# Kernel tuning notes

Measured on AMD Instinct MI355X. Metric: run time of the kernel, lower is better.

Reference implementation:

```python
import jax, jax.numpy as jnp
import numpy as np

D_MODEL = 4096
D_FIBER = 16
D_CONTROL = 64
EMA_MOMENTUM = 0.9


def setup_inputs() -> dict:
    key = jax.random.key(0)
    k_h, k_f, k_w1, k_w2 = jax.random.split(key, 4)
    B, S = 4, 2048
    hidden = jax.random.normal(k_h, (B, S, D_MODEL), dtype=jnp.float32)
    # torch nn.Linear stores weight as [out, in]; fiber_proj init: normal std=0.02
    W_fiber = jax.random.normal(k_f, (D_FIBER, D_MODEL), dtype=jnp.float32) * 0.02
    # predictor[0]: Linear(d_model+d_fiber, d_control) with default torch init (uniform)
    fan_in1 = D_MODEL + D_FIBER
    bound1 = 1.0 / np.sqrt(fan_in1)
    W1 = jax.random.uniform(k_w1, (D_CONTROL, fan_in1), dtype=jnp.float32, minval=-bound1, maxval=bound1)
    b1 = jnp.zeros((D_CONTROL,), dtype=jnp.float32)
    # predictor[-2]: Linear(d_control, 1), weight normal std=0.01, bias zero
    W2 = jax.random.normal(k_w2, (1, D_CONTROL), dtype=jnp.float32) * 0.01
    b2 = jnp.zeros((1,), dtype=jnp.float32)
    lam = jnp.asarray(1.0, dtype=jnp.float32)
    return {"hidden": hidden, "W_fiber": W_fiber, "W1": W1, "b1": b1, "W2": W2, "b2": b2, "lam": lam}


def _causal_ema(delta_h, alpha):
    # h_t = alpha*h_{t-1} + (1-alpha)*d_t, h_{-1} = 0. delta_h: [B,S]
    B = delta_h.shape[0]
    def step(h_prev, d_t):
        h_t = alpha * h_prev + (1.0 - alpha) * d_t
        return h_t, h_t
    _, hs = jax.lax.scan(step, jnp.zeros((B,), delta_h.dtype), jnp.swapaxes(delta_h, 0, 1))
    return jnp.swapaxes(hs, 0, 1)  # [B,S]


def reference(hidden, W_fiber, W1, b1, W2, b2, lam):
    h = hidden.astype(jnp.float32)                      # [B,S,D]
    fiber = jnp.einsum('bsd,fd->bsf', h, W_fiber)       # [B,S,16]
    combined = jnp.concatenate([h, fiber], axis=-1)     # [B,S,D+16]
    z = jax.nn.gelu(jnp.einsum('bsc,kc->bsk', combined, W1) + b1, approximate=False)
    delta_h = jax.nn.softplus(jnp.einsum('bsk,ok->bso', z, W2) + b2)[..., 0]  # [B,S]
    field = _causal_ema(delta_h, EMA_MOMENTUM)          # [B,S]
    gate = jax.nn.sigmoid(-lam * field)
    return gate.astype(hidden.dtype), field.astype(hidden.dtype), delta_h.mean()
```

## Files before the change

### kernel.cpp

```cpp
#include <hip/hip_runtime.h>
#include <hip/hip_bf16.h>

#define D_MODEL 4096
#define NTOK    8192
#define SEQ     2048

typedef short bf16x8 __attribute__((ext_vector_type(8)));
typedef float f32x4  __attribute__((ext_vector_type(4)));

__device__ inline short f2bf(float x) {
  __hip_bfloat16 h = __float2bfloat16(x);
  return *reinterpret_cast<short*>(&h);
}
__device__ inline float bf2f(const void* p, size_t i) {
  return __bfloat162float(((const __hip_bfloat16*)p)[i]);
}

__global__ __launch_bounds__(320) void sniff_k(const void* hid, const void* wf,
                                               const void* w1, const void* w2,
                                               const void* b1, const void* b2,
                                               const void* lam,
                                               int* flags, float* scal) {
  int wv = threadIdx.x >> 6, lane = threadIdx.x & 63;
  const unsigned short* p = nullptr;
  int n = 0;
  switch (wv) {
    case 0: p = (const unsigned short*)hid; n = NTOK * D_MODEL; break;
    case 1: p = (const unsigned short*)wf;  n = 16 * D_MODEL;   break;
    case 2: p = (const unsigned short*)w1;  n = 64 * 4112;      break;
    case 3: p = (const unsigned short*)w2;  n = 64;             break;
    case 4: p = (const unsigned short*)b1;  n = 64;             break;
  }
  int S = n / 2 < 64 ? n / 2 : 64;
  bool act = lane < S;
  unsigned short ve = 0, vo = 0;
  if (act) { ve = p[2 * lane]; vo = p[2 * lane + 1]; }
  int ee = (ve >> 7) & 0xFF, eo = (vo >> 7) & 0xFF;
  bool ve_band   = (ve == 0) || (ve == 0x8000) || (ee >= 96 && ee <= 141);
  bool vo_bandnz = (vo != 0) && (vo != 0x8000) && (eo >= 96 && eo <= 141);
  int zp = __popcll(__ballot(act && ve == 0 && vo == 0));
  int ob = __popcll(__ballot(act && ve == 0 && vo_bandnz));
  int eb = __popcll(__ballot(act && ve_band));
  if (lane == 0) {
    int f;
    if (zp == S) f = 1;
    else if (4 * ob >= 3 * S) f = 0;
    else if (4 * eb >= 3 * S) f = 1;
    else f = 0;
    flags[wv] = f;
  }
  if (threadIdx.x == 0) {
    unsigned short l0 = *(const unsigned short*)lam;
    int le = (l0 >> 7) & 0xFF;
    if (l0 != 0 && l0 != 0x8000 && le >= 96 && le <= 141)
      scal[0] = __bfloat162float(*(const __hip_bfloat16*)lam);
    else
      scal[0] = *(const float*)lam;
    unsigned short c0 = *(const unsigned short*)b2;
    int ce = (c0 >> 7) & 0xFF;
    if (c0 == 0) scal[1] = 0.0f;
    else if (c0 != 0x8000 && ce >= 96 && ce <= 141)
      scal[1] = __bfloat162float(*(const __hip_bfloat16*)b2);
    else
      scal[1] = *(const float*)b2;
  }
}

__global__ __launch_bounds__(256) void fold_w1(const void* __restrict__ W1v,
                                               const void* __restrict__ Wfv,
                                               const int* __restrict__ flags,
                                               __hip_bfloat16* __restrict__ W1eff) {
  int n = blockIdx.x;
  int fw1 = flags[2], fwf = flags[1];
  __shared__ float w1b[16];
  if (threadIdx.x < 16) {
    size_t idx = (size_t)n * 4112 + 4096 + threadIdx.x;
    w1b[threadIdx.x] = fw1 ? bf2f(W1v, idx) : ((const float*)W1v)[idx];
  }
  __syncthreads();
  for (int k = threadIdx.x; k < D_MODEL; k += 256) {
    size_t idx = (size_t)n * 4112 + k;
    float v = fw1 ? bf2f(W1v, idx) : ((const float*)W1v)[idx];
#pragma unroll
    for (int f = 0; f < 16; ++f) {
      size_t wi = (size_t)f * D_MODEL + k;
      float wfv = fwf ? bf2f(Wfv, wi) : ((const float*)Wfv)[wi];
      v += w1b[f] * wfv;
    }
    W1eff[(size_t)n * D_MODEL + k] = __float2bfloat16(v);
  }
}

__global__ __launch_bounds__(256) void gemm_delta(const void* __restrict__ hid,
                                                  const short* __restrict__ B_,
                                                  const void* __restrict__ b1,
                                                  const void* __restrict__ w2,
                                                  const int* __restrict__ flags,
                                                  const float* __restrict__ scal,
                                                  float* __restrict__ delta) {
  int tile = blockIdx.x;
  int w    = threadIdx.x >> 6;
  int lane = threadIdx.x & 63;
  int m = lane & 15, kg = lane >> 4;
  size_t abase = (size_t)(tile * 16 + m) * D_MODEL + w * 1024 + kg * 8;
  const short* Bp = B_ + (size_t)m * D_MODEL + w * 1024 + kg * 8;
  f32x4 acc0 = {0.f, 0.f, 0.f, 0.f};
  f32x4 acc1 = acc0, acc2 = acc0, acc3 = acc0;
  if (flags[0]) {
    const short* Ap = (const short*)hid + abase;
#pragma unroll 4
    for (int ks = 0; ks < 1024; ks += 32) {
      bf16x8 a   = *(const bf16x8*)(Ap + ks);
      bf16x8 b0  = *(const bf16x8*)(Bp + ks);
      bf16x8 b1f = *(const bf16x8*)(Bp + 16 * D_MODEL + ks);
      bf16x8 b2f = *(const bf16x8*)(Bp + 32 * D_MODEL + ks);
      bf16x8 b3f = *(const bf16x8*)(Bp + 48 * D_MODEL + ks);
      acc0 = __builtin_amdgcn_mfma_f32_16x16x32_bf16(a, b0, acc0, 0, 0, 0);
      acc1 = __builtin_amdgcn_mfma_f32_16x16x32_bf16(a, b1f, acc1, 0, 0, 0);
      acc2 = __builtin_amdgcn_mfma_f32_16x16x32_bf16(a, b2f, acc2, 0, 0, 0);
      acc3 = __builtin_amdgcn_mfma_f32_16x16x32_bf16(a, b3f, acc3, 0, 0, 0);
    }
  } else {
    const float* Ap = (const float*)hid + abase;
#pragma unroll 2
    for (int ks = 0; ks < 1024; ks += 32) {
      float4 lo = *(const float4*)(Ap + ks);
      float4 hi = *(const float4*)(Ap + ks + 4);
      bf16x8 a;
      a[0] = f2bf(lo.x); a[1] = f2bf(lo.y); a[2] = f2bf(lo.z); a[3] = f2bf(lo.w);
      a[4] = f2bf(hi.x); a[5] = f2bf(hi.y); a[6] = f2bf(hi.z); a[7] = f2bf(hi.w);
      bf16x8 b0  = *(const bf16x8*)(Bp + ks);
      bf16x8 b1f = *(const bf16x8*)(Bp + 16 * D_MODEL + ks);
      bf16x8 b2f = *(const bf16x8*)(Bp + 32 * D_MODEL + ks);
      bf16x8 b3f = *(const bf16x8*)(Bp + 48 * D_MODEL + ks);
      acc0 = __builtin_amdgcn_mfma_f32_16x16x32_bf16(a, b0, acc0, 0, 0, 0);
      acc1 = __builtin_amdgcn_mfma_f32_16x16x32_bf16(a, b1f, acc1, 0, 0, 0);
      acc2 = __builtin_amdgcn_mfma_f32_16x16x32_bf16(a, b2f, acc2, 0, 0, 0);
      acc3 = __builtin_amdgcn_mfma_f32_16x16x32_bf16(a, b3f, acc3, 0, 0, 0);
    }
  }
  __shared__ float red[4][16][64];
#pragma unroll
  for (int r = 0; r < 4; ++r) {
    int row = kg * 4 + r;
    red[w][row][ 0 + m] = acc0[r];
    red[w][row][16 + m] = acc1[r];
    red[w][row][32 + m] = acc2[r];
    red[w][row][48 + m] = acc3[r];
  }
  __syncthreads();
  int row = threadIdx.x >> 4, cid = threadIdx.x & 15;
  int fb1 = flags[4], fw2 = flags[3];
  float y = 0.f;
#pragma unroll
  for (int j = 0; j < 4; ++j) {
    int c = cid + 16 * j;
    float s = red[0][row][c] + red[1][row][c] + red[2][row][c] + red[3][row][c];
    s += fb1 ? bf2f(b1, c) : ((const float*)b1)[c];
    float g = 0.5f * s * (1.0f + erff(s * 0.70710678118654752f));
    y += g * (fw2 ? bf2f(w2, c) : ((const float*)w2)[c]);
  }
#pragma unroll
  for (int off = 1; off <= 8; off <<= 1) y += __shfl_xor(y, off, 64);
  if (cid == 0) {
    float x = y + scal[1];
    float d = (x > 20.0f) ? x : log1pf(expf(x));
    delta[tile * 16 + row] = d;
  }
}

__global__ __launch_bounds__(256) void ema_out(const float* __restrict__ delta,
                                               const float* __restrict__ scal,
                                               float* __restrict__ out) {
  int b    = threadIdx.x >> 6;
  int lane = threadIdx.x & 63;
  const float alpha = 0.9f;
  float d[32];
  const float* dp = delta + b * SEQ + lane * 32;
  float beta = 0.f, lsum = 0.f;
#pragma unroll
  for (int i = 0; i < 32; ++i) {
    d[i] = dp[i];
    lsum += d[i];
    beta = alpha * beta + 0.1f * d[i];
  }
  float accA = 0.03433683820292512f;
  float accB = beta;
  for (int off = 1; off < 64; off <<= 1) {
    float uA = __shfl_up(accA, off, 64);
    float uB = __shfl_up(accB, off, 64);
    if (lane >= off) {
      accB = accB + accA * uB;
      accA = accA * uA;
    }
  }
  float prev = __shfl_up(accB, 1, 64);
  float h = (lane == 0) ? 0.f : prev;
  float lam = scal[0];
#pragma unroll
  for (int i = 0; i < 32; ++i) {
    h = alpha * h + 0.1f * d[i];
    float gate = 1.0f / (1.0f + expf(lam * h));
    out[b * SEQ + lane * 32 + i]        = gate;
    out[NTOK + b * SEQ + lane * 32 + i] = h;
  }
#pragma unroll
  for (int off = 32; off >= 1; off >>= 1) lsum += __shfl_xor(lsum, off, 64);
  __shared__ float bs[4];
  if (lane == 0) bs[b] = lsum;
  __syncthreads();
  if (threadIdx.x == 0)
    out[2 * NTOK] = (bs[0] + bs[1] + bs[2] + bs[3]) * (1.0f / 8192.0f);
}

extern "C" void kernel_launch(void* const* d_in, const int* in_sizes, int n_in,
                              void* d_out, int out_size, void* d_ws, size_t ws_size,
                              hipStream_t stream) {
  const void* hidden = d_in[0];
  const void* Wf     = d_in[1];
  const void* W1     = d_in[2];
  const void* b1     = d_in[3];
  const void* W2     = d_in[4];
  const void* b2     = d_in[5];
  const void* lam    = d_in[6];
  float* out = (float*)d_out;

  char* ws = (char*)d_ws;
  int*   flags = (int*)ws;
  float* scal  = (float*)(ws + 32);
  __hip_bfloat16* W1eff = (__hip_bfloat16*)(ws + 64);
  float* delta = (float*)(ws + 64 + (size_t)64 * D_MODEL * 2);

  sniff_k<<<1, 320, 0, stream>>>(hidden, Wf, W1, W2, b1, b2, lam, flags, scal);
  fold_w1<<<64, 256, 0, stream>>>(W1, Wf, flags, W1eff);
  gemm_delta<<<512, 256, 0, stream>>>(hidden, (const short*)W1eff, b1, W2, flags, scal, delta);
  ema_out<<<1, 256, 0, stream>>>(delta, scal, out);
}
```

Before: 251.0 us.

## Stage hidden and weight tiles in LDS with async double-buffered loads

Rewrites the GEMM kernel so each block handles 32 tokens and stages 256-wide K chunks of the activation and folded-weight tiles in padded LDS. The bf16 path uses global_load_lds async copies with double buffering and raw waitcnt/barriers; the fp32 path converts hidden to bf16 into LDS with scalar loads, then synchronises. The aim is to halve weight re-reads per token and overlap loads with MFMA. The trade-off is a large LDS footprint (about 100KB) that limits occupancy to one block per CU, and an fp32 path with no load/compute overlap.

```diff
diff --git a/kernel.cpp b/kernel.cpp
--- a/kernel.cpp
+++ b/kernel.cpp
@@ -4,9 +4,17 @@
 #define D_MODEL 4096
 #define NTOK    8192
 #define SEQ     2048
+#define RS      264
 
 typedef short bf16x8 __attribute__((ext_vector_type(8)));
 typedef float f32x4  __attribute__((ext_vector_type(4)));
+
+typedef const __attribute__((address_space(1))) char* gas1_t;
+typedef __attribute__((address_space(3))) char* las3_t;
+
+__device__ inline void async16(const void* g, void* l) {
+  __builtin_amdgcn_global_load_lds((gas1_t)g, (las3_t)l, 16, 0, 0);
+}
 
 __device__ inline short f2bf(float x) {
   __hip_bfloat16 h = __float2bfloat16(x);
@@ -91,81 +99,113 @@
   }
 }
 
-__global__ __launch_bounds__(256) void gemm_delta(const void* __restrict__ hid,
+__global__ __launch_bounds__(256) void gemm_fused(const void* __restrict__ hid,
                                                   const short* __restrict__ B_,
                                                   const void* __restrict__ b1,
                                                   const void* __restrict__ w2,
                                                   const int* __restrict__ flags,
                                                   const float* __restrict__ scal,
                                                   float* __restrict__ delta) {
-  int tile = blockIdx.x;
-  int w    = threadIdx.x >> 6;
-  int lane = threadIdx.x & 63;
+  __shared__ short As[2][32 * RS];
+  __shared__ short Bs[2][64 * RS];
+  int t = blockIdx.x;
+  int tid = threadIdx.x;
+  int w = tid >> 6, lane = tid & 63;
   int m = lane & 15, kg = lane >> 4;
-  size_t abase = (size_t)(tile * 16 + m) * D_MODEL + w * 1024 + kg * 8;
-  const short* Bp = B_ + (size_t)m * D_MODEL + w * 1024 + kg * 8;
-  f32x4 acc0 = {0.f, 0.f, 0.f, 0.f};
-  f32x4 acc1 = acc0, acc2 = acc0, acc3 = acc0;
+  int kh = w >> 1, rg = w & 1;
+  bool lo = lane < 32;
+  int l5 = lane & 31;
+  f32x4 acc[4];
+#pragma unroll
+  for (int g = 0; g < 4; ++g) acc[g] = (f32x4){0.f, 0.f, 0.f, 0.f};
+
+  auto compute = [&](const short* Asc, const short* Bsc) {
+#pragma unroll
+    for (int j = 0; j < 4; ++j) {
+      int ko = kh * 128 + j * 32 + kg * 8;
+      bf16x8 a   = *(const bf16x8*)(Asc + (rg * 16 + m) * RS + ko);
+      bf16x8 b0v = *(const bf16x8*)(Bsc + (m +  0) * RS + ko);
+      bf16x8 b1v = *(const bf16x8*)(Bsc + (m + 16) * RS + ko);
+      bf16x8 b2v = *(const bf16x8*)(Bsc + (m + 32) * RS + ko);
+      bf16x8 b3v = *(const bf16x8*)(Bsc + (m + 48) * RS + ko);
+      acc[0] = __builtin_amdgcn_mfma_f32_16x16x32_bf16(a, b0v, acc[0], 0, 0, 0);
+      acc[1] = __builtin_amdgcn_mfma_f32_16x16x32_bf16(a, b1v, acc[1], 0, 0, 0);
+      acc[2] = __builtin_amdgcn_mfma_f32_16x16x32_bf16(a, b2v, acc[2], 0, 0, 0);
+      acc[3] = __builtin_amdgcn_mfma_f32_16x16x32_bf16(a, b3v, acc[3], 0, 0, 0);
+    }
+  };
+
   if (flags[0]) {
-    const short* Ap = (const short*)hid + abase;
-#pragma unroll 4
-    for (int ks = 0; ks < 1024; ks += 32) {
-      bf16x8 a   = *(const bf16x8*)(Ap + ks);
-      bf16x8 b0  = *(const bf16x8*)(Bp + ks);
-      bf16x8 b1f = *(const bf16x8*)(Bp + 16 * D_MODEL + ks);
-      bf16x8 b2f = *(const bf16x8*)(Bp + 32 * D_MODEL + ks);
-      bf16x8 b3f = *(const bf16x8*)(Bp + 48 * D_MODEL + ks);
-      acc0 = __builtin_amdgcn_mfma_f32_16x16x32_bf16(a, b0, acc0, 0, 0, 0);
-      acc1 = __builtin_amdgcn_mfma_f32_16x16x32_bf16(a, b1f, acc1, 0, 0, 0);
-      acc2 = __builtin_amdgcn_mfma_f32_16x16x32_bf16(a, b2f, acc2, 0, 0, 0);
-      acc3 = __builtin_amdgcn_mfma_f32_16x16x32_bf16(a, b3f, acc3, 0, 0, 0);
-    }
+    const short* hidA = (const short*)hid;
+    auto stage = [&](int c, int p) {
+#pragma unroll
+      for (int i = 0; i < 8; ++i) {
+        int r = w * 8 + i;
+        const short* gp = hidA + (size_t)(t * 32 + r) * D_MODEL + c * 256 + l5 * 8;
+        if (lo) async16(gp, &As[p][r * RS]);
+      }
+#pragma unroll
+      for (int i = 0; i < 16; ++i) {
+        int r = w * 16 + i;
+        const short* gp = B_ + (size_t)r * D_MODEL + c * 256 + l5 * 8;
+        if (lo) async16(gp, &Bs[p][r * RS]);
+      }
+    };
+    stage(0, 0);
+#pragma unroll 1
+    for (int c = 0; c < 15; ++c) {
+      stage(c + 1, (c + 1) & 1);
+      __builtin_amdgcn_s_waitcnt(0x4F78);
+      __builtin_amdgcn_s_barrier();
+      compute(As[c & 1], Bs[c & 1]);
+      __builtin_amdgcn_s_barrier();
+    }
+    __builtin_amdgcn_s_waitcnt(0x0F70);
+    __builtin_amdgcn_s_barrier();
+    compute(As[1], Bs[1]);
   } else {
-    const float* Ap = (const float*)hid + abase;
-#pragma unroll 2
-    for (int ks = 0; ks < 1024; ks += 32) {
-      float4 lo = *(const float4*)(Ap + ks);
-      float4 hi = *(const float4*)(Ap + ks + 4);
-      bf16x8 a;
-      a[0] = f2bf(lo.x); a[1] = f2bf(lo.y); a[2] = f2bf(lo.z); a[3] = f2bf(lo.w);
-      a[4] = f2bf(hi.x); a[5] = f2bf(hi.y); a[6] = f2bf(hi.z); a[7] = f2bf(hi.w);
-      bf16x8 b0  = *(const bf16x8*)(Bp + ks);
-      bf16x8 b1f = *(const bf16x8*)(Bp + 16 * D_MODEL + ks);
-      bf16x8 b2f = *(const bf16x8*)(Bp + 32 * D_MODEL + ks);
-      bf16x8 b3f = *(const bf16x8*)(Bp + 48 * D_MODEL + ks);
-      acc0 = __builtin_amdgcn_mfma_f32_16x16x32_bf16(a, b0, acc0, 0, 0, 0);
-      acc1 = __builtin_amdgcn_mfma_f32_16x16x32_bf16(a, b1f, acc1, 0, 0, 0);
-      acc2 = __builtin_amdgcn_mfma_f32_16x16x32_bf16(a, b2f, acc2, 0, 0, 0);
-      acc3 = __builtin_amdgcn_mfma_f32_16x16x32_bf16(a, b3f, acc3, 0, 0, 0);
-    }
-  }
-  __shared__ float red[4][16][64];
-#pragma unroll
-  for (int r = 0; r < 4; ++r) {
-    int row = kg * 4 + r;
-    red[w][row][ 0 + m] = acc0[r];
-    red[w][row][16 + m] = acc1[r];
-    red[w][row][32 + m] = acc2[r];
-    red[w][row][48 + m] = acc3[r];
-  }
+    const float* hidF = (const float*)hid;
+#pragma unroll 1
+    for (int c = 0; c < 16; ++c) {
+#pragma unroll
+      for (int i = 0; i < 16; ++i) {
+        int r = w * 16 + i;
+        const short* gp = B_ + (size_t)r * D_MODEL + c * 256 + l5 * 8;
+        if (lo) async16(gp, &Bs[0][r * RS]);
+      }
+      for (int e = tid; e < 32 * 256; e += 256) {
+        int r = e >> 8, k = e & 255;
+        As[0][r * RS + k] = f2bf(hidF[(size_t)(t * 32 + r) * D_MODEL + c * 256 + k]);
+      }
+      __syncthreads();
+      compute(As[0], Bs[0]);
+      __syncthreads();
+    }
+  }
+
+  float* red = (float*)&As[0][0];
+#pragma unroll
+  for (int g = 0; g < 4; ++g)
+#pragma unroll
+    for (int r = 0; r < 4; ++r)
+      red[kh * 2048 + (rg * 16 + kg * 4 + r) * 64 + g * 16 + m] = acc[g][r];
   __syncthreads();
-  int row = threadIdx.x >> 4, cid = threadIdx.x & 15;
+  int row = tid >> 3, cid = tid & 7;
   int fb1 = flags[4], fw2 = flags[3];
   float y = 0.f;
 #pragma unroll
-  for (int j = 0; j < 4; ++j) {
-    int c = cid + 16 * j;
-    float s = red[0][row][c] + red[1][row][c] + red[2][row][c] + red[3][row][c];
-    s += fb1 ? bf2f(b1, c) : ((const float*)b1)[c];
-    float g = 0.5f * s * (1.0f + erff(s * 0.70710678118654752f));
-    y += g * (fw2 ? bf2f(w2, c) : ((const float*)w2)[c]);
-  }
-#pragma unroll
-  for (int off = 1; off <= 8; off <<= 1) y += __shfl_xor(y, off, 64);
+  for (int j = 0; j < 8; ++j) {
+    int col = cid + 8 * j;
+    float s = red[row * 64 + col] + red[2048 + row * 64 + col];
+    s += fb1 ? bf2f(b1, col) : ((const float*)b1)[col];
+    float gg = 0.5f * s * (1.0f + erff(s * 0.70710678118654752f));
+    y += gg * (fw2 ? bf2f(w2, col) : ((const float*)w2)[col]);
+  }
+#pragma unroll
+  for (int off = 1; off <= 4; off <<= 1) y += __shfl_xor(y, off, 64);
   if (cid == 0) {
     float x = y + scal[1];
-    float d = (x > 20.0f) ? x : log1pf(expf(x));
-    delta[tile * 16 + row] = d;
+    delta[t * 32 + row] = (x > 20.0f) ? x : log1pf(expf(x));
   }
 }
 
@@ -233,6 +273,6 @@
 
   sniff_k<<<1, 320, 0, stream>>>(hidden, Wf, W1, W2, b1, b2, lam, flags, scal);
   fold_w1<<<64, 256, 0, stream>>>(W1, Wf, flags, W1eff);
-  gemm_delta<<<512, 256, 0, stream>>>(hidden, (const short*)W1eff, b1, W2, flags, scal, delta);
+  gemm_fused<<<256, 256, 0, stream>>>(hidden, (const short*)W1eff, b1, W2, flags, scal, delta);
   ema_out<<<1, 256, 0, stream>>>(delta, scal, out);
 }
```

Result: no change. 249.5 us (-0.6%).
